# Kernel tuning notes

Hardware: AMD Instinct MI355X
Metric: run time of the kernel (lower is better)

The kernel has to match this reference:

```python
import jax, jax.numpy as jnp
import numpy as np

B, S, D, K = 128, 200, 128, 4
NQ, NC = 10000, 500


def setup_inputs() -> dict:
    key = jax.random.key(0)
    ks = jax.random.split(key, 20)
    f = jnp.float32
    inp = {}
    inp["question_seq"] = jax.random.randint(ks[0], (B, S), 0, NQ)
    inp["hint_attempt_seq"] = jax.random.randint(ks[1], (B, S), 0, 12)
    inp["correct_seq"] = jax.random.randint(ks[2], (B, S), 0, 2)
    inp["interval_time_seq"] = jax.random.randint(ks[3], (B, S), 0, 100)
    inp["use_time_seq"] = jax.random.randint(ks[4], (B, S), 0, 100)
    inp["q2c_table"] = jax.random.randint(ks[5], (NQ, K), 0, NC)
    inp["q2c_mask_table"] = jax.random.randint(ks[6], (NQ, K), 0, 2)
    s = 0.1
    inp["embed_question"] = jax.random.normal(ks[7], (NQ, D), f) * s
    inp["embed_question_disc"] = jax.random.normal(ks[8], (NQ, 1), f) * s
    inp["embed_concept"] = jax.random.normal(ks[9], (NC, D), f) * s
    inp["embed_interval_time"] = jax.random.normal(ks[10], (100, D), f) * s
    inp["embed_use_time"] = jax.random.normal(ks[11], (100, D), f) * s
    inp["embed_hint_attempt"] = jax.random.normal(ks[12], (12, D), f) * s
    inp["W_fuse"] = jax.random.normal(ks[13], (2 * D, D), f) / np.float32(np.sqrt(2 * D))
    inp["b_fuse"] = jnp.zeros((D,), f)
    inp["W_absorb"] = jax.random.normal(ks[14], (3 * D, D), f) / np.float32(np.sqrt(3 * D))
    inp["b_absorb"] = jnp.zeros((D,), f)
    inp["W_forget"] = jax.random.normal(ks[15], (3 * D, D), f) / np.float32(np.sqrt(3 * D))
    inp["b_forget"] = jnp.zeros((D,), f)
    inp["latent0"] = jax.random.normal(ks[16], (B, D), f) * 0.1  # xavier-init latent_pre
    return inp


def _cos(a, b, eps=1e-8):
    # torch.cosine_similarity semantics with eps clamp on each norm
    num = jnp.sum(a * b, axis=-1)
    na = jnp.sqrt(jnp.sum(a * a, axis=-1))
    nb = jnp.sqrt(jnp.sum(b * b, axis=-1))
    return num / (jnp.maximum(na, eps) * jnp.maximum(nb, eps))


def _forward(question_seq, hint_attempt_seq, correct_seq, interval_time_seq, use_time_seq,
             q2c_table, q2c_mask_table,
             embed_question, embed_question_disc, embed_concept, embed_interval_time,
             embed_use_time, embed_hint_attempt,
             W_fuse, b_fuse, W_absorb, b_absorb, W_forget, b_forget, latent0):
    f = latent0.dtype
    qe = embed_question[question_seq]                                # [B,S,D]
    qd = jax.nn.sigmoid(embed_question_disc[question_seq]) * 10.0    # [B,S,1]
    ce = jnp.broadcast_to(correct_seq.astype(f)[:, :, None], qe.shape)  # [B,S,D]
    ite = embed_interval_time[interval_time_seq]                     # [B,S,D]
    ute = embed_use_time[use_time_seq]                               # [B,S,D]
    hae = embed_hint_attempt[hint_attempt_seq]                       # [B,S,D]
    cp = embed_concept[q2c_table[question_seq]]                      # [B,S,K,D]
    m = q2c_mask_table[question_seq].astype(f)                       # [B,S,K]

    tm = lambda x: jnp.swapaxes(x, 0, 1)  # time-major for scan
    xs = (tm(qe[:, :-1]), tm(ce[:, :-1]), tm(ute[:, :-1]), tm(hae[:, :-1]), tm(ite[:, :-1]),
          tm(cp[:, :-1]), tm(cp[:, 1:]), tm(qd[:, 1:]), tm(m[:, :-1]))

    def step(lp, x):
        qe_t, ce_t, ute_t, hae_t, ite_t, cp_t, cp_t1, qd_t1, m_t = x
        inter = jnp.concatenate([qe_t, ce_t], axis=-1) @ W_fuse + b_fuse
        absorb = jnp.concatenate([inter, ute_t, hae_t], axis=-1) @ W_absorb + b_absorb
        forget = jax.nn.sigmoid(jnp.concatenate([lp, ite_t, inter], axis=-1) @ W_forget + b_forget)
        lc = lp * forget + absorb  # dropout p=0 -> identity
        qdiff = (_cos(qe_t[:, None, :], cp_t) + 1.0) * 0.5   # [B,K]
        uab = (_cos(lc[:, None, :], cp_t1) + 1.0) * 0.5      # [B,K]
        logit = qd_t1[:, 0] * jnp.sum((uab - qdiff) * m_t, axis=-1)  # [B]
        return lc, jax.nn.sigmoid(logit)

    _, ys = jax.lax.scan(step, latent0, xs)  # ys: [S-1, B]
    y = jnp.concatenate([ys.T, jnp.zeros((latent0.shape[0], 1), f)], axis=1)  # [B,S], last col 0
    return y


def reference(question_seq, hint_attempt_seq, correct_seq, interval_time_seq, use_time_seq,
              q2c_table, q2c_mask_table,
              embed_question, embed_question_disc, embed_concept, embed_interval_time,
              embed_use_time, embed_hint_attempt,
              W_fuse, b_fuse, W_absorb, b_absorb, W_forget, b_forget, latent0):
    return _forward(question_seq, hint_attempt_seq, correct_seq, interval_time_seq, use_time_seq,
                    q2c_table, q2c_mask_table,
                    embed_question, embed_question_disc, embed_concept, embed_interval_time,
                    embed_use_time, embed_hint_attempt,
                    W_fuse, b_fuse, W_absorb, b_absorb, W_forget, b_forget, latent0)
```

## Files before the change

### kernel.cpp

```cpp
#include <hip/hip_runtime.h>
#include <hip/hip_bf16.h>

typedef unsigned short u16;

#define Bb  128
#define Ss  200
#define Tt  199
#define NQq 10000
#define NCc 500
#define CHK 16
#define NCH 13

__device__ inline float bf2f(u16 u) {
    union { unsigned int i; float f; } x;
    x.i = ((unsigned int)u) << 16;
    return x.f;
}

__device__ inline float ldf(const void* p, int i, int m) {
    if (m) return ((const float*)p)[i];
    return bf2f(((const u16*)p)[i]);
}

__device__ inline void stf(void* p, int i, int m, float v) {
    if (m) ((float*)p)[i] = v;
    else ((__hip_bfloat16*)p)[i] = __float2bfloat16(v);
}

__device__ inline int clampi(int v, int lo, int hi) {
    return v < lo ? lo : (v > hi ? hi : v);
}

__device__ inline float wave_red(float v) {
#pragma unroll
    for (int m = 32; m >= 1; m >>= 1) v += __shfl_xor(v, m);
    return v;
}

__device__ inline float4 f4add(float4 a, float4 b) {
    return make_float4(a.x + b.x, a.y + b.y, a.z + b.z, a.w + b.w);
}
__device__ inline float4 f4fma(float s, float4 a, float4 b) {
    return make_float4(fmaf(s, a.x, b.x), fmaf(s, a.y, b.y),
                       fmaf(s, a.z, b.z), fmaf(s, a.w, b.w));
}

__device__ inline int detect_mode(const void* Eq) {
    const u16* q = (const u16*)Eq;
    const int l = threadIdx.x & 63;
    float mx = 0.f;
#pragma unroll
    for (int k = 0; k < 4; ++k) {
        float a = fabsf(bf2f(q[l * 4 + k]));
        if (!(a == a)) a = 3.0e38f;
        mx = fmaxf(mx, a);
    }
#pragma unroll
    for (int s = 32; s >= 1; s >>= 1) mx = fmaxf(mx, __shfl_xor(mx, s));
    return (mx > 1.0e6f) ? 1 : 0;
}

__global__ __launch_bounds__(256) void k_prep(
    const void* Eq, const void* Eqd, const void* Wf, const void* Wa, const void* Wg,
    const void* bfu, const void* ba, const void* bg,
    const void* Eut, const void* Eha, const void* Eit, const void* Ec,
    const int* q2c, const int* q2cm,
    float* BabT, float* BfgT,
    float* vA0, float* vA1, float* vF0, float* vF1,
    float* PA_ut, float* PA_ha, float* PF_it, float* qdm, float* qd10) {
    const int m = detect_mode(Eq);
    const int job = blockIdx.x, tid = threadIdx.x;
    __shared__ float cs2s[128];
    if (job < 128) {
        const int r = job, col = tid & 127;
        float acc = 0.f;
        if (tid < 128) {
            for (int j = 0; j < 128; ++j)
                acc += ldf(Wf, r * 128 + j, m) * ldf(Wa, j * 128 + col, m);
            BabT[r * 128 + col] = acc;
        } else {
            for (int j = 0; j < 128; ++j)
                acc += ldf(Wf, r * 128 + j, m) * ldf(Wg, (256 + j) * 128 + col, m);
            BfgT[r * 128 + col] = acc;
        }
    } else if (job == 128) {
        const int col = tid & 127;
        if (tid < 128) {
            float s = 0.f;
            for (int r2 = 0; r2 < 128; ++r2) s += ldf(Wf, (128 + r2) * 128 + col, m);
            cs2s[col] = s;
        }
        __syncthreads();
        float a0 = 0.f, a1 = 0.f;
        if (tid < 128) {
            for (int j = 0; j < 128; ++j) {
                const float wv = ldf(Wa, j * 128 + col, m);
                a0 += ldf(bfu, j, m) * wv;
                a1 += cs2s[j] * wv;
            }
            vA0[col] = a0 + ldf(ba, col, m);
            vA1[col] = a1;
        } else {
            for (int j = 0; j < 128; ++j) {
                const float wv = ldf(Wg, (256 + j) * 128 + col, m);
                a0 += ldf(bfu, j, m) * wv;
                a1 += cs2s[j] * wv;
            }
            vF0[col] = a0 + ldf(bg, col, m);
            vF1[col] = a1;
        }
    } else if (job < 229) {
        const int r = job - 129, col = tid & 127;
        float acc = 0.f;
        if (tid < 128) {
            for (int j = 0; j < 128; ++j)
                acc += ldf(Eut, r * 128 + j, m) * ldf(Wa, (128 + j) * 128 + col, m);
            PA_ut[r * 128 + col] = acc;
        } else {
            for (int j = 0; j < 128; ++j)
                acc += ldf(Eit, r * 128 + j, m) * ldf(Wg, (128 + j) * 128 + col, m);
            PF_it[r * 128 + col] = acc;
        }
    } else if (job < 241) {
        const int r = job - 229;
        if (tid < 128) {
            float acc = 0.f;
            for (int j = 0; j < 128; ++j)
                acc += ldf(Eha, r * 128 + j, m) * ldf(Wa, (256 + j) * 128 + tid, m);
            PA_ha[r * 128 + tid] = acc;
        }
    } else {
        const int wv = tid >> 6, lane = tid & 63;
        const int q = (job - 241) * 4 + wv;
        const float qa = ldf(Eq, q * 128 + lane, m);
        const float qb = ldf(Eq, q * 128 + 64 + lane, m);
        const float nqc = fmaxf(sqrtf(wave_red(qa * qa + qb * qb)), 1e-8f);
        const int4 cc = ((const int4*)q2c)[q];
        const int4 mm = ((const int4*)q2cm)[q];
        const int cks[4] = {clampi(cc.x, 0, NCc - 1), clampi(cc.y, 0, NCc - 1),
                            clampi(cc.z, 0, NCc - 1), clampi(cc.w, 0, NCc - 1)};
        const int ms[4]  = {mm.x, mm.y, mm.z, mm.w};
        float qs = 0.f;
#pragma unroll
        for (int k = 0; k < 4; ++k) {
            const int ck = cks[k];
            const float ea = ldf(Ec, ck * 128 + lane, m);
            const float eb = ldf(Ec, ck * 128 + 64 + lane, m);
            const float dot = wave_red(qa * ea + qb * eb);
            const float nn = fmaxf(sqrtf(wave_red(ea * ea + eb * eb)), 1e-8f);
            qs += (float)ms[k] * (0.5f * dot / (nqc * nn) + 0.5f);
        }
        if (lane == 0) {
            qdm[q] = qs;
            qd10[q] = 10.f / (1.f + __expf(-ldf(Eqd, q, m)));
        }
    }
}

__global__ __launch_bounds__(256) void k_gemm(
    const void* Eq, const float* BabT, const float* BfgT,
    float* PA_q, float* PF_q) {
    const int m = detect_mode(Eq);
    const int tid = threadIdx.x;
    __shared__ float At[32][36];
    __shared__ float Bt0[32][128];
    __shared__ float Bt1[32][128];
    const int r0 = blockIdx.x * 32;
    float acc0[2][8], acc1[2][8];
#pragma unroll
    for (int j = 0; j < 2; ++j)
#pragma unroll
        for (int i = 0; i < 8; ++i) { acc0[j][i] = 0.f; acc1[j][i] = 0.f; }
    const int tx = tid & 15, ty = tid >> 4;
    for (int ks = 0; ks < 4; ++ks) {
        {
            const int row = tid >> 3, seg = tid & 7;
            const int q = clampi(r0 + row, 0, NQq - 1);
            const int ei = q * 128 + ks * 32 + seg * 4;
            float* dst = &At[row][seg * 4];
            if (m) {
                float4 v = *(const float4*)((const float*)Eq + ei);
                dst[0] = v.x; dst[1] = v.y; dst[2] = v.z; dst[3] = v.w;
            } else {
                uint2 v = *(const uint2*)((const u16*)Eq + ei);
                dst[0] = bf2f((u16)(v.x & 0xffff)); dst[1] = bf2f((u16)(v.x >> 16));
                dst[2] = bf2f((u16)(v.y & 0xffff)); dst[3] = bf2f((u16)(v.y >> 16));
            }
        }
        {
            const float4* s0 = (const float4*)(BabT + ks * 32 * 128);
            const float4* s1 = (const float4*)(BfgT + ks * 32 * 128);
            float4* d0 = (float4*)&Bt0[0][0];
            float4* d1 = (float4*)&Bt1[0][0];
#pragma unroll
            for (int k = 0; k < 4; ++k) {
                d0[tid + k * 256] = s0[tid + k * 256];
                d1[tid + k * 256] = s1[tid + k * 256];
            }
        }
        __syncthreads();
#pragma unroll
        for (int kk = 0; kk < 32; kk += 4) {
            float a_[2][4];
            *(float4*)&a_[0][0] = *(const float4*)&At[ty * 2 + 0][kk];
            *(float4*)&a_[1][0] = *(const float4*)&At[ty * 2 + 1][kk];
#pragma unroll
            for (int q = 0; q < 4; ++q) {
                float4 b0 = *(const float4*)&Bt0[kk + q][tx * 8];
                float4 b1 = *(const float4*)&Bt0[kk + q][tx * 8 + 4];
                float4 c0 = *(const float4*)&Bt1[kk + q][tx * 8];
                float4 c1 = *(const float4*)&Bt1[kk + q][tx * 8 + 4];
#pragma unroll
                for (int j = 0; j < 2; ++j) {
                    const float av = a_[j][q];
                    acc0[j][0] += av * b0.x; acc0[j][1] += av * b0.y;
                    acc0[j][2] += av * b0.z; acc0[j][3] += av * b0.w;
                    acc0[j][4] += av * b1.x; acc0[j][5] += av * b1.y;
                    acc0[j][6] += av * b1.z; acc0[j][7] += av * b1.w;
                    acc1[j][0] += av * c0.x; acc1[j][1] += av * c0.y;
                    acc1[j][2] += av * c0.z; acc1[j][3] += av * c0.w;
                    acc1[j][4] += av * c1.x; acc1[j][5] += av * c1.y;
                    acc1[j][6] += av * c1.z; acc1[j][7] += av * c1.w;
                }
            }
        }
        __syncthreads();
    }
#pragma unroll
    for (int j = 0; j < 2; ++j) {
        const int q = r0 + ty * 2 + j;
        if (q < NQq) {
            float* oa = PA_q + q * 128 + tx * 8;
            float* of = PF_q + q * 128 + tx * 8;
#pragma unroll
            for (int i = 0; i < 8; ++i) { oa[i] = acc0[j][i]; of[i] = acc1[j][i]; }
        }
    }
}

__global__ __launch_bounds__(256) void p4_scan(
    const int* q_seq, const int* ut_seq, const int* ha_seq, const int* it_seq,
    const int* c_seq,
    const void* Eq, const void* Wg, const void* L0,
    const float* PA_q, const float* PA_ut, const float* PA_ha,
    const float* PF_q, const float* PF_it,
    const float* vA0, const float* vA1, const float* vF0, const float* vF1,
    float* lc_seq) {
    const int m = detect_mode(Eq);
    const int b = blockIdx.x;
    const int tid = threadIdx.x;
    const int wv = tid >> 6, l = tid & 63;
    const int d0 = 2 * l;
    const int ib = wv << 5;
    const int dd = ib + (l & 31);

    __shared__ float part[2][4][128];
    __shared__ float st_ab[CHK * 128];
    __shared__ float st_pf[CHK * 128];

    float wA[32], wB[32];
#pragma unroll
    for (int k = 0; k < 32; ++k) {
        wA[k] = ldf(Wg, (ib + k) * 128 + d0, m);
        wB[k] = ldf(Wg, (ib + k) * 128 + d0 + 1, m);
    }
    float lc = (l < 32) ? ldf(L0, b * 128 + dd, m) : 0.f;

    const int srow = tid >> 4, seg = tid & 15;
    const int off8 = seg * 8;
    const float4 A0a = *(const float4*)(vA0 + off8), A0b = *(const float4*)(vA0 + off8 + 4);
    const float4 A1a = *(const float4*)(vA1 + off8), A1b = *(const float4*)(vA1 + off8 + 4);
    const float4 F0a = *(const float4*)(vF0 + off8), F0b = *(const float4*)(vF0 + off8 + 4);
    const float4 F1a = *(const float4*)(vF1 + off8), F1b = *(const float4*)(vF1 + off8 + 4);

    float4 qa0, qa1, ua0, ua1, ga0, ga1, qf0, qf1, if0, if1;
    float cf;
#define LOAD_CHUNK(C)                                                          \
    {                                                                          \
        int tt = (C) * CHK + srow; if (tt > Tt - 1) tt = Tt - 1;               \
        const int base = b * Ss + tt;                                          \
        const int qt = clampi(q_seq[base], 0, NQq - 1);                        \
        const int ut = clampi(ut_seq[base], 0, 99);                            \
        const int ha = clampi(ha_seq[base], 0, 11);                            \
        const int it = clampi(it_seq[base], 0, 99);                            \
        cf = (float)c_seq[base];                                               \
        const float* pq = PA_q + qt * 128 + off8;                              \
        qa0 = *(const float4*)pq; qa1 = *(const float4*)(pq + 4);              \
        const float* pu = PA_ut + ut * 128 + off8;                             \
        ua0 = *(const float4*)pu; ua1 = *(const float4*)(pu + 4);              \
        const float* ph = PA_ha + ha * 128 + off8;                             \
        ga0 = *(const float4*)ph; ga1 = *(const float4*)(ph + 4);              \
        const float* pf = PF_q + qt * 128 + off8;                              \
        qf0 = *(const float4*)pf; qf1 = *(const float4*)(pf + 4);              \
        const float* pi = PF_it + it * 128 + off8;                             \
        if0 = *(const float4*)pi; if1 = *(const float4*)(pi + 4);              \
    }

    LOAD_CHUNK(0)
    float lcbuf[CHK];
    int par = 0;

    for (int c = 0; c < NCH; ++c) {
        __syncthreads();
        {
            float4 ab0 = f4fma(cf, A1a, f4add(f4add(qa0, ua0), f4add(ga0, A0a)));
            float4 ab1 = f4fma(cf, A1b, f4add(f4add(qa1, ua1), f4add(ga1, A0b)));
            float4 pf0 = f4fma(cf, F1a, f4add(qf0, f4add(if0, F0a)));
            float4 pf1 = f4fma(cf, F1b, f4add(qf1, f4add(if1, F0b)));
            float4* sa = (float4*)(st_ab + srow * 128 + off8);
            sa[0] = ab0; sa[1] = ab1;
            float4* sp = (float4*)(st_pf + srow * 128 + off8);
            sp[0] = pf0; sp[1] = pf1;
        }
        __syncthreads();

        float abr = 0.f, pfr = 0.f;
        if (l < 32) { abr = st_ab[dd]; pfr = st_pf[dd]; }

#pragma unroll
        for (int s = 0; s < CHK; ++s) {
            float pa0 = 0.f, pa1 = 0.f, pb0 = 0.f, pb1 = 0.f;
#pragma unroll
            for (int k = 0; k < 32; k += 2) {
                const float u0 = __uint_as_float(
                    __builtin_amdgcn_readlane(__float_as_uint(lc), k));
                const float u1 = __uint_as_float(
                    __builtin_amdgcn_readlane(__float_as_uint(lc), k + 1));
                pa0 = fmaf(u0, wA[k], pa0);
                pb0 = fmaf(u0, wB[k], pb0);
                pa1 = fmaf(u1, wA[k + 1], pa1);
                pb1 = fmaf(u1, wB[k + 1], pb1);
            }
            *(float2*)&part[par][wv][d0] = make_float2(pa0 + pa1, pb0 + pb1);
            if (s == 1 && c + 1 < NCH) LOAD_CHUNK(c + 1)
            __syncthreads();
            if (l < 32) {
                const float fs = part[par][0][dd] + part[par][1][dd]
                               + part[par][2][dd] + part[par][3][dd];
                const float fg = 1.f / (1.f + __expf(-(fs + pfr)));
                lc = lc * fg + abr;
                lcbuf[s] = lc;
                if (s + 1 < CHK) {
                    abr = st_ab[((s + 1) << 7) + dd];
                    pfr = st_pf[((s + 1) << 7) + dd];
                }
            }
            par ^= 1;
        }
        if (l < 32) {
#pragma unroll
            for (int s = 0; s < CHK; ++s) {
                const int t = c * CHK + s;
                if (t < Tt)
                    lc_seq[((long)t * 128 + b) * 128 + dd] = lcbuf[s];
            }
        }
    }
#undef LOAD_CHUNK
}

__global__ __launch_bounds__(256) void p5_out(
    const int* q_seq, const int* q2c, const int* q2cm,
    const float* lc_seq, const float* qdm, const float* qd10,
    const void* Eq, const void* Ec, void* out) {
    const int m = detect_mode(Eq);
    const int wv = threadIdx.x >> 6, lane = threadIdx.x & 63;
    const int r = blockIdx.x * 4 + wv;
    const int t = r >> 7, b = r & 127;
    const int qt  = clampi(q_seq[b * Ss + t], 0, NQq - 1);
    const int qt1 = clampi(q_seq[b * Ss + t + 1], 0, NQq - 1);
    const int4 mm = ((const int4*)q2cm)[qt];
    int4 ci = ((const int4*)q2c)[qt1];
    const int c0 = clampi(ci.x, 0, NCc - 1), c1 = clampi(ci.y, 0, NCc - 1);
    const int c2 = clampi(ci.z, 0, NCc - 1), c3 = clampi(ci.w, 0, NCc - 1);
    const float la = lc_seq[(long)r * 128 + lane];
    const float lb = lc_seq[(long)r * 128 + 64 + lane];
    const float e0a = ldf(Ec, c0 * 128 + lane, m), e0b = ldf(Ec, c0 * 128 + 64 + lane, m);
    const float e1a = ldf(Ec, c1 * 128 + lane, m), e1b = ldf(Ec, c1 * 128 + 64 + lane, m);
    const float e2a = ldf(Ec, c2 * 128 + lane, m), e2b = ldf(Ec, c2 * 128 + 64 + lane, m);
    const float e3a = ldf(Ec, c3 * 128 + lane, m), e3b = ldf(Ec, c3 * 128 + 64 + lane, m);
    float nl = la * la + lb * lb;
    float d0 = la * e0a + lb * e0b, n0 = e0a * e0a + e0b * e0b;
    float d1 = la * e1a + lb * e1b, n1 = e1a * e1a + e1b * e1b;
    float d2 = la * e2a + lb * e2b, n2 = e2a * e2a + e2b * e2b;
    float d3 = la * e3a + lb * e3b, n3 = e3a * e3a + e3b * e3b;
#pragma unroll
    for (int s = 32; s >= 1; s >>= 1) {
        nl += __shfl_xor(nl, s);
        d0 += __shfl_xor(d0, s); d1 += __shfl_xor(d1, s);
        d2 += __shfl_xor(d2, s); d3 += __shfl_xor(d3, s);
        n0 += __shfl_xor(n0, s); n1 += __shfl_xor(n1, s);
        n2 += __shfl_xor(n2, s); n3 += __shfl_xor(n3, s);
    }
    if (lane == 0) {
        const float inl = 1.f / fmaxf(sqrtf(nl), 1e-8f);
        const float accv =
              (float)mm.x * (0.5f * d0 * inl / fmaxf(sqrtf(n0), 1e-8f) + 0.5f)
            + (float)mm.y * (0.5f * d1 * inl / fmaxf(sqrtf(n1), 1e-8f) + 0.5f)
            + (float)mm.z * (0.5f * d2 * inl / fmaxf(sqrtf(n2), 1e-8f) + 0.5f)
            + (float)mm.w * (0.5f * d3 * inl / fmaxf(sqrtf(n3), 1e-8f) + 0.5f);
        const float logit = qd10[qt1] * (accv - qdm[qt]);
        stf(out, b * Ss + t, m, 1.f / (1.f + __expf(-logit)));
        if (t == 0) stf(out, b * Ss + 199, m, 0.f);
    }
}

extern "C" void kernel_launch(void* const* d_in, const int* in_sizes, int n_in,
                              void* d_out, int out_size, void* d_ws, size_t ws_size,
                              hipStream_t stream) {
    (void)in_sizes; (void)n_in; (void)out_size; (void)ws_size;
    const int* q_seq  = (const int*)d_in[0];
    const int* ha_seq = (const int*)d_in[1];
    const int* c_seq  = (const int*)d_in[2];
    const int* it_seq = (const int*)d_in[3];
    const int* ut_seq = (const int*)d_in[4];
    const int* q2c    = (const int*)d_in[5];
    const int* q2cm   = (const int*)d_in[6];
    const void* Eq   = d_in[7];
    const void* Eqd  = d_in[8];
    const void* Ec   = d_in[9];
    const void* Eit  = d_in[10];
    const void* Eut  = d_in[11];
    const void* Eha  = d_in[12];
    const void* Wf   = d_in[13];
    const void* bfu  = d_in[14];
    const void* Wa   = d_in[15];
    const void* ba   = d_in[16];
    const void* Wg   = d_in[17];
    const void* bg   = d_in[18];
    const void* L0   = d_in[19];

    float* ws    = (float*)d_ws;
    float* vA0   = ws;
    float* vA1   = vA0 + 128;
    float* vF0   = vA1 + 128;
    float* vF1   = vF0 + 128;
    float* BabT  = vF1 + 128;
    float* BfgT  = BabT + 16384;
    float* PA_ut = BfgT + 16384;
    float* PA_ha = PA_ut + 12800;
    float* PF_it = PA_ha + 1536;
    float* qdm   = PF_it + 12800;
    float* qd10  = qdm + 10016;
    float* PA_q  = qd10 + 10016;
    float* PF_q  = PA_q + 1280000;
    float* lc_seq= PF_q + 1280000;

    hipLaunchKernelGGL(k_prep, dim3(2741), dim3(256), 0, stream,
                       Eq, Eqd, Wf, Wa, Wg, bfu, ba, bg, Eut, Eha, Eit, Ec,
                       q2c, q2cm, BabT, BfgT, vA0, vA1, vF0, vF1,
                       PA_ut, PA_ha, PF_it, qdm, qd10);
    hipLaunchKernelGGL(k_gemm, dim3(313), dim3(256), 0, stream,
                       Eq, BabT, BfgT, PA_q, PF_q);
    hipLaunchKernelGGL(p4_scan, dim3(Bb), dim3(256), 0, stream,
                       q_seq, ut_seq, ha_seq, it_seq, c_seq, Eq, Wg, L0,
                       PA_q, PA_ut, PA_ha, PF_q, PF_it,
                       vA0, vA1, vF0, vF1, lc_seq);
    hipLaunchKernelGGL(p5_out, dim3(Tt * Bb / 4), dim3(256), 0, stream,
                       q_seq, q2c, q2cm, lc_seq, qdm, qd10, Eq, Ec, d_out);
}
```

Baseline: 247.0 us.

## Fuse question GEMM into prep kernel as two-stage matmul, simplify scan step

The separate k_gemm launch is removed. Each of the first 313 prep blocks now computes Eq·Wf for 32 rows into shared memory and then multiplies by Wa and Wg directly, so the precomputed BabT/BfgT products no longer need a global round trip. This drops one launch and its dependency on the prep blocks, but doubles the GEMM FLOPs and raises shared-memory use per block, which lowers occupancy for every prep job. The scan kernel also issues the next-chunk load before the step loop, reads ab/pf from shared memory inside each step, and folds the two-way split FMA chains into one chain.

```diff
diff --git a/kernel.cpp b/kernel.cpp
--- a/kernel.cpp
+++ b/kernel.cpp
@@ -60,35 +60,151 @@
     return (mx > 1.0e6f) ? 1 : 0;
 }
 
+__device__ inline void load_tile_4096(float* dst, const void* src, int base,
+                                      int tid, int m) {
+    if (m) {
+        const float4* s = (const float4*)((const float*)src + base);
+        float4* d = (float4*)dst;
+#pragma unroll
+        for (int k = 0; k < 4; ++k) d[tid + k * 256] = s[tid + k * 256];
+    } else {
+        const u16* s = (const u16*)src + base;
+#pragma unroll
+        for (int k = 0; k < 4; ++k) {
+            const int idx = (tid + k * 256) * 4;
+            uint2 v = *(const uint2*)(s + idx);
+            float* d = dst + idx;
+            d[0] = bf2f((u16)(v.x & 0xffff)); d[1] = bf2f((u16)(v.x >> 16));
+            d[2] = bf2f((u16)(v.y & 0xffff)); d[3] = bf2f((u16)(v.y >> 16));
+        }
+    }
+}
+
 __global__ __launch_bounds__(256) void k_prep(
     const void* Eq, const void* Eqd, const void* Wf, const void* Wa, const void* Wg,
     const void* bfu, const void* ba, const void* bg,
     const void* Eut, const void* Eha, const void* Eit, const void* Ec,
     const int* q2c, const int* q2cm,
-    float* BabT, float* BfgT,
     float* vA0, float* vA1, float* vF0, float* vF1,
-    float* PA_ut, float* PA_ha, float* PF_it, float* qdm, float* qd10) {
+    float* PA_ut, float* PA_ha, float* PF_it, float* qdm, float* qd10,
+    float* PA_q, float* PF_q) {
     const int m = detect_mode(Eq);
     const int job = blockIdx.x, tid = threadIdx.x;
-    __shared__ float cs2s[128];
-    if (job < 128) {
-        const int r = job, col = tid & 127;
-        float acc = 0.f;
-        if (tid < 128) {
-            for (int j = 0; j < 128; ++j)
-                acc += ldf(Wf, r * 128 + j, m) * ldf(Wa, j * 128 + col, m);
-            BabT[r * 128 + col] = acc;
-        } else {
-            for (int j = 0; j < 128; ++j)
-                acc += ldf(Wf, r * 128 + j, m) * ldf(Wg, (256 + j) * 128 + col, m);
-            BfgT[r * 128 + col] = acc;
-        }
-    } else if (job == 128) {
+    __shared__ __align__(16) float smem[12416];
+    if (job < 313) {
+        float* t32s = smem;
+        float* At   = smem + 4224;
+        float* BtW  = smem + 5376;
+        float* Bt0  = smem + 4224;
+        float* Bt1  = smem + 8320;
+        const int r0 = job * 32;
+        const int tx = tid & 15, ty = tid >> 4;
+        float accT[2][8];
+#pragma unroll
+        for (int j = 0; j < 2; ++j)
+#pragma unroll
+            for (int i = 0; i < 8; ++i) accT[j][i] = 0.f;
+        for (int ks = 0; ks < 4; ++ks) {
+            {
+                const int row = tid >> 3, seg = tid & 7;
+                const int q = clampi(r0 + row, 0, NQq - 1);
+                const int ei = q * 128 + ks * 32 + seg * 4;
+                float* dst = At + row * 36 + seg * 4;
+                if (m) {
+                    float4 v = *(const float4*)((const float*)Eq + ei);
+                    dst[0] = v.x; dst[1] = v.y; dst[2] = v.z; dst[3] = v.w;
+                } else {
+                    uint2 v = *(const uint2*)((const u16*)Eq + ei);
+                    dst[0] = bf2f((u16)(v.x & 0xffff)); dst[1] = bf2f((u16)(v.x >> 16));
+                    dst[2] = bf2f((u16)(v.y & 0xffff)); dst[3] = bf2f((u16)(v.y >> 16));
+                }
+            }
+            load_tile_4096(BtW, Wf, ks * 32 * 128, tid, m);
+            __syncthreads();
+#pragma unroll
+            for (int kk = 0; kk < 32; kk += 4) {
+                float a_[2][4];
+                *(float4*)&a_[0][0] = *(const float4*)(At + (ty * 2 + 0) * 36 + kk);
+                *(float4*)&a_[1][0] = *(const float4*)(At + (ty * 2 + 1) * 36 + kk);
+#pragma unroll
+                for (int q4 = 0; q4 < 4; ++q4) {
+                    float4 b0 = *(const float4*)(BtW + (kk + q4) * 128 + tx * 8);
+                    float4 b1 = *(const float4*)(BtW + (kk + q4) * 128 + tx * 8 + 4);
+#pragma unroll
+                    for (int j = 0; j < 2; ++j) {
+                        const float av = a_[j][q4];
+                        accT[j][0] += av * b0.x; accT[j][1] += av * b0.y;
+                        accT[j][2] += av * b0.z; accT[j][3] += av * b0.w;
+                        accT[j][4] += av * b1.x; accT[j][5] += av * b1.y;
+                        accT[j][6] += av * b1.z; accT[j][7] += av * b1.w;
+                    }
+                }
+            }
+            __syncthreads();
+        }
+#pragma unroll
+        for (int j = 0; j < 2; ++j) {
+            const int row = ty * 2 + j;
+            *(float4*)(t32s + row * 132 + tx * 8) =
+                make_float4(accT[j][0], accT[j][1], accT[j][2], accT[j][3]);
+            *(float4*)(t32s + row * 132 + tx * 8 + 4) =
+                make_float4(accT[j][4], accT[j][5], accT[j][6], accT[j][7]);
+        }
+        __syncthreads();
+        float acc0[2][8], acc1[2][8];
+#pragma unroll
+        for (int j = 0; j < 2; ++j)
+#pragma unroll
+            for (int i = 0; i < 8; ++i) { acc0[j][i] = 0.f; acc1[j][i] = 0.f; }
+        for (int ks2 = 0; ks2 < 4; ++ks2) {
+            load_tile_4096(Bt0, Wa, ks2 * 32 * 128, tid, m);
+            load_tile_4096(Bt1, Wg, 256 * 128 + ks2 * 32 * 128, tid, m);
+            __syncthreads();
+#pragma unroll
+            for (int kk = 0; kk < 32; kk += 4) {
+                float a_[2][4];
+                *(float4*)&a_[0][0] =
+                    *(const float4*)(t32s + (ty * 2 + 0) * 132 + ks2 * 32 + kk);
+                *(float4*)&a_[1][0] =
+                    *(const float4*)(t32s + (ty * 2 + 1) * 132 + ks2 * 32 + kk);
+#pragma unroll
+                for (int q4 = 0; q4 < 4; ++q4) {
+                    float4 b0 = *(const float4*)(Bt0 + (kk + q4) * 128 + tx * 8);
+                    float4 b1 = *(const float4*)(Bt0 + (kk + q4) * 128 + tx * 8 + 4);
+                    float4 c0 = *(const float4*)(Bt1 + (kk + q4) * 128 + tx * 8);
+                    float4 c1 = *(const float4*)(Bt1 + (kk + q4) * 128 + tx * 8 + 4);
+#pragma unroll
+                    for (int j = 0; j < 2; ++j) {
+                        const float av = a_[j][q4];
+                        acc0[j][0] += av * b0.x; acc0[j][1] += av * b0.y;
+                        acc0[j][2] += av * b0.z; acc0[j][3] += av * b0.w;
+                        acc0[j][4] += av * b1.x; acc0[j][5] += av * b1.y;
+                        acc0[j][6] += av * b1.z; acc0[j][7] += av * b1.w;
+                        acc1[j][0] += av * c0.x; acc1[j][1] += av * c0.y;
+                        acc1[j][2] += av * c0.z; acc1[j][3] += av * c0.w;
+                        acc1[j][4] += av * c1.x; acc1[j][5] += av * c1.y;
+                        acc1[j][6] += av * c1.z; acc1[j][7] += av * c1.w;
+                    }
+                }
+            }
+            __syncthreads();
+        }
+#pragma unroll
+        for (int j = 0; j < 2; ++j) {
+            const int q = r0 + ty * 2 + j;
+            if (q < NQq) {
+                float* oa = PA_q + q * 128 + tx * 8;
+                float* of = PF_q + q * 128 + tx * 8;
+#pragma unroll
+                for (int i = 0; i < 8; ++i) { oa[i] = acc0[j][i]; of[i] = acc1[j][i]; }
+            }
+        }
+    } else if (job == 313) {
         const int col = tid & 127;
         if (tid < 128) {
             float s = 0.f;
             for (int r2 = 0; r2 < 128; ++r2) s += ldf(Wf, (128 + r2) * 128 + col, m);
-            cs2s[col] = s;
+            smem[col] = s;
         }
         __syncthreads();
         float a0 = 0.f, a1 = 0.f;
@@ -96,7 +212,7 @@
             for (int j = 0; j < 128; ++j) {
                 const float wv = ldf(Wa, j * 128 + col, m);
                 a0 += ldf(bfu, j, m) * wv;
-                a1 += cs2s[j] * wv;
+                a1 += smem[j] * wv;
             }
             vA0[col] = a0 + ldf(ba, col, m);
             vA1[col] = a1;
@@ -104,13 +220,13 @@
             for (int j = 0; j < 128; ++j) {
                 const float wv = ldf(Wg, (256 + j) * 128 + col, m);
                 a0 += ldf(bfu, j, m) * wv;
-                a1 += cs2s[j] * wv;
+                a1 += smem[j] * wv;
             }
             vF0[col] = a0 + ldf(bg, col, m);
             vF1[col] = a1;
         }
-    } else if (job < 229) {
-        const int r = job - 129, col = tid & 127;
+    } else if (job < 414) {
+        const int r = job - 314, col = tid & 127;
         float acc = 0.f;
         if (tid < 128) {
             for (int j = 0; j < 128; ++j)
@@ -121,8 +237,8 @@
                 acc += ldf(Eit, r * 128 + j, m) * ldf(Wg, (128 + j) * 128 + col, m);
             PF_it[r * 128 + col] = acc;
         }
-    } else if (job < 241) {
-        const int r = job - 229;
+    } else if (job < 426) {
+        const int r = job - 414;
         if (tid < 128) {
             float acc = 0.f;
             for (int j = 0; j < 128; ++j)
@@ -131,7 +247,7 @@
         }
     } else {
         const int wv = tid >> 6, lane = tid & 63;
-        const int q = (job - 241) * 4 + wv;
+        const int q = (job - 426) * 4 + wv;
         const float qa = ldf(Eq, q * 128 + lane, m);
         const float qb = ldf(Eq, q * 128 + 64 + lane, m);
         const float nqc = fmaxf(sqrtf(wave_red(qa * qa + qb * qb)), 1e-8f);
@@ -153,87 +269,6 @@
         if (lane == 0) {
             qdm[q] = qs;
             qd10[q] = 10.f / (1.f + __expf(-ldf(Eqd, q, m)));
-        }
-    }
-}
-
-__global__ __launch_bounds__(256) void k_gemm(
-    const void* Eq, const float* BabT, const float* BfgT,
-    float* PA_q, float* PF_q) {
-    const int m = detect_mode(Eq);
-    const int tid = threadIdx.x;
-    __shared__ float At[32][36];
-    __shared__ float Bt0[32][128];
-    __shared__ float Bt1[32][128];
-    const int r0 = blockIdx.x * 32;
-    float acc0[2][8], acc1[2][8];
-#pragma unroll
-    for (int j = 0; j < 2; ++j)
-#pragma unroll
-        for (int i = 0; i < 8; ++i) { acc0[j][i] = 0.f; acc1[j][i] = 0.f; }
-    const int tx = tid & 15, ty = tid >> 4;
-    for (int ks = 0; ks < 4; ++ks) {
-        {
-            const int row = tid >> 3, seg = tid & 7;
-            const int q = clampi(r0 + row, 0, NQq - 1);
-            const int ei = q * 128 + ks * 32 + seg * 4;
-            float* dst = &At[row][seg * 4];
-            if (m) {
-                float4 v = *(const float4*)((const float*)Eq + ei);
-                dst[0] = v.x; dst[1] = v.y; dst[2] = v.z; dst[3] = v.w;
-            } else {
-                uint2 v = *(const uint2*)((const u16*)Eq + ei);
-                dst[0] = bf2f((u16)(v.x & 0xffff)); dst[1] = bf2f((u16)(v.x >> 16));
-                dst[2] = bf2f((u16)(v.y & 0xffff)); dst[3] = bf2f((u16)(v.y >> 16));
-            }
-        }
-        {
-            const float4* s0 = (const float4*)(BabT + ks * 32 * 128);
-            const float4* s1 = (const float4*)(BfgT + ks * 32 * 128);
-            float4* d0 = (float4*)&Bt0[0][0];
-            float4* d1 = (float4*)&Bt1[0][0];
-#pragma unroll
-            for (int k = 0; k < 4; ++k) {
-                d0[tid + k * 256] = s0[tid + k * 256];
-                d1[tid + k * 256] = s1[tid + k * 256];
-            }
-        }
-        __syncthreads();
-#pragma unroll
-        for (int kk = 0; kk < 32; kk += 4) {
-            float a_[2][4];
-            *(float4*)&a_[0][0] = *(const float4*)&At[ty * 2 + 0][kk];
-            *(float4*)&a_[1][0] = *(const float4*)&At[ty * 2 + 1][kk];
-#pragma unroll
-            for (int q = 0; q < 4; ++q) {
-                float4 b0 = *(const float4*)&Bt0[kk + q][tx * 8];
-                float4 b1 = *(const float4*)&Bt0[kk + q][tx * 8 + 4];
-                float4 c0 = *(const float4*)&Bt1[kk + q][tx * 8];
-                float4 c1 = *(const float4*)&Bt1[kk + q][tx * 8 + 4];
-#pragma unroll
-                for (int j = 0; j < 2; ++j) {
-                    const float av = a_[j][q];
-                    acc0[j][0] += av * b0.x; acc0[j][1] += av * b0.y;
-                    acc0[j][2] += av * b0.z; acc0[j][3] += av * b0.w;
-                    acc0[j][4] += av * b1.x; acc0[j][5] += av * b1.y;
-                    acc0[j][6] += av * b1.z; acc0[j][7] += av * b1.w;
-                    acc1[j][0] += av * c0.x; acc1[j][1] += av * c0.y;
-                    acc1[j][2] += av * c0.z; acc1[j][3] += av * c0.w;
-                    acc1[j][4] += av * c1.x; acc1[j][5] += av * c1.y;
-                    acc1[j][6] += av * c1.z; acc1[j][7] += av * c1.w;
-                }
-            }
-        }
-        __syncthreads();
-    }
-#pragma unroll
-    for (int j = 0; j < 2; ++j) {
-        const int q = r0 + ty * 2 + j;
-        if (q < NQq) {
-            float* oa = PA_q + q * 128 + tx * 8;
-            float* of = PF_q + q * 128 + tx * 8;
-#pragma unroll
-            for (int i = 0; i < 8; ++i) { oa[i] = acc0[j][i]; of[i] = acc1[j][i]; }
         }
     }
 }
@@ -312,38 +347,29 @@
             float4* sp = (float4*)(st_pf + srow * 128 + off8);
             sp[0] = pf0; sp[1] = pf1;
         }
+        if (c + 1 < NCH) LOAD_CHUNK(c + 1)
         __syncthreads();
 
-        float abr = 0.f, pfr = 0.f;
-        if (l < 32) { abr = st_ab[dd]; pfr = st_pf[dd]; }
-
 #pragma unroll
         for (int s = 0; s < CHK; ++s) {
-            float pa0 = 0.f, pa1 = 0.f, pb0 = 0.f, pb1 = 0.f;
-#pragma unroll
-            for (int k = 0; k < 32; k += 2) {
-                const float u0 = __uint_as_float(
+            float pa = 0.f, pb = 0.f;
+#pragma unroll
+            for (int k = 0; k < 32; ++k) {
+                const float u = __uint_as_float(
                     __builtin_amdgcn_readlane(__float_as_uint(lc), k));
-                const float u1 = __uint_as_float(
-                    __builtin_amdgcn_readlane(__float_as_uint(lc), k + 1));
-                pa0 = fmaf(u0, wA[k], pa0);
-                pb0 = fmaf(u0, wB[k], pb0);
-                pa1 = fmaf(u1, wA[k + 1], pa1);
-                pb1 = fmaf(u1, wB[k + 1], pb1);
-            }
-            *(float2*)&part[par][wv][d0] = make_float2(pa0 + pa1, pb0 + pb1);
-            if (s == 1 && c + 1 < NCH) LOAD_CHUNK(c + 1)
+                pa = fmaf(u, wA[k], pa);
+                pb = fmaf(u, wB[k], pb);
+            }
+            *(float2*)&part[par][wv][d0] = make_float2(pa, pb);
             __syncthreads();
             if (l < 32) {
                 const float fs = part[par][0][dd] + part[par][1][dd]
                                + part[par][2][dd] + part[par][3][dd];
-                const float fg = 1.f / (1.f + __expf(-(fs + pfr)));
-                lc = lc * fg + abr;
+                const float ab = st_ab[(s << 7) + dd];
+                const float pf = st_pf[(s << 7) + dd];
+                const float fg = 1.f / (1.f + __expf(-(fs + pf)));
+                lc = lc * fg + ab;
                 lcbuf[s] = lc;
-                if (s + 1 < CHK) {
-                    abr = st_ab[((s + 1) << 7) + dd];
-                    pfr = st_pf[((s + 1) << 7) + dd];
-                }
             }
             par ^= 1;
         }
@@ -435,9 +461,7 @@
     float* vA1   = vA0 + 128;
     float* vF0   = vA1 + 128;
     float* vF1   = vF0 + 128;
-    float* BabT  = vF1 + 128;
-    float* BfgT  = BabT + 16384;
-    float* PA_ut = BfgT + 16384;
+    float* PA_ut = vF1 + 128;
     float* PA_ha = PA_ut + 12800;
     float* PF_it = PA_ha + 1536;
     float* qdm   = PF_it + 12800;
@@ -446,12 +470,10 @@
     float* PF_q  = PA_q + 1280000;
     float* lc_seq= PF_q + 1280000;
 
-    hipLaunchKernelGGL(k_prep, dim3(2741), dim3(256), 0, stream,
+    hipLaunchKernelGGL(k_prep, dim3(2926), dim3(256), 0, stream,
                        Eq, Eqd, Wf, Wa, Wg, bfu, ba, bg, Eut, Eha, Eit, Ec,
-                       q2c, q2cm, BabT, BfgT, vA0, vA1, vF0, vF1,
-                       PA_ut, PA_ha, PF_it, qdm, qd10);
-    hipLaunchKernelGGL(k_gemm, dim3(313), dim3(256), 0, stream,
-                       Eq, BabT, BfgT, PA_q, PF_q);
+                       q2c, q2cm, vA0, vA1, vF0, vF1,
+                       PA_ut, PA_ha, PF_it, qdm, qd10, PA_q, PF_q);
     hipLaunchKernelGGL(p4_scan, dim3(Bb), dim3(256), 0, stream,
                        q_seq, ut_seq, ha_seq, it_seq, c_seq, Eq, Wg, L0,
                        PA_q, PA_ut, PA_ha, PF_q, PF_it,
```

After: 230.2 us. 1.07x faster.
